# Optimization experiments

Measured on AMD Instinct MI355X. Metric: run time of the kernel, lower is better.

## Reference

```python
import jax, jax.numpy as jnp
import numpy as np

SEQ, D_A, H, D_K, D_V = 4096, 2048, 16, 128, 128


def setup_inputs() -> dict:
    key = jax.random.key(0)
    ks = jax.random.split(key, 7)
    return {
        "queries": jax.random.normal(ks[0], (SEQ, D_A), dtype=jnp.float32),
        "keys":    jax.random.normal(ks[1], (SEQ, D_A), dtype=jnp.float32),
        "values":  jax.random.normal(ks[2], (SEQ, D_A), dtype=jnp.float32),
        "Eq": jax.random.normal(ks[3], (H, D_A, D_K), dtype=jnp.float32),
        "Ek": jax.random.normal(ks[4], (H, D_A, D_K), dtype=jnp.float32),
        "Ev": jax.random.normal(ks[5], (H, D_A, D_V), dtype=jnp.float32),
        "W_out": jax.random.normal(ks[6], (H * D_V, D_A), dtype=jnp.float32),
    }


def reference(queries, keys, values, Eq, Ek, Ev, W_out):
    # Per-head projections: [seq, d_a] x [h, d_a, d] -> [h, seq, d]
    Q = jnp.einsum("sd,hdk->hsk", queries, Eq)
    K = jnp.einsum("sd,hdk->hsk", keys, Ek)
    V = jnp.einsum("sd,hdv->hsv", values, Ev)
    scale = 1.0 / D_K  # faithful to source: 1/d_k, not 1/sqrt(d_k)
    dots = jnp.einsum("hqk,hsk->hqs", Q, K) * scale  # [h, seq, seq]
    attn = jax.nn.softmax(dots, axis=-1)  # dropout p=0 -> identity
    out = jnp.einsum("hqs,hsv->hqv", attn, V)  # [h, seq, d_v]
    # concat heads along last dim: [seq, h*d_v]
    A = jnp.transpose(out, (1, 0, 2)).reshape(SEQ, H * D_V)
    return A @ W_out  # [seq, d_a]
```

## Files before the change

kernel.cpp:

```cpp
#include <hip/hip_runtime.h>

typedef unsigned short u16;
typedef __attribute__((ext_vector_type(4)))  float  f32x4;
typedef __attribute__((ext_vector_type(16))) float  f32x16;
typedef __attribute__((ext_vector_type(4)))  float  float4v;
typedef __attribute__((ext_vector_type(4)))  unsigned short u16x4;
typedef __attribute__((ext_vector_type(8)))  unsigned short u16x8;
typedef __attribute__((ext_vector_type(8)))  short s16x8;
typedef __attribute__((ext_vector_type(4)))  unsigned int u32x4;

#define SEQ 4096
#define DA  2048
#define NH  16
#define DKV 128

__device__ __forceinline__ u16 f2bf(float f) {
    unsigned u = __builtin_bit_cast(unsigned, f);
    u += 0x7FFFu + ((u >> 16) & 1u);
    return (u16)(u >> 16);
}
__device__ __forceinline__ float bf2f(u16 h) {
    return __builtin_bit_cast(float, (unsigned)h << 16);
}
__device__ __forceinline__ f32x4 mfma16(u16x8 a, u16x8 b, f32x4 c) {
    return __builtin_amdgcn_mfma_f32_16x16x32_bf16(
        __builtin_bit_cast(s16x8, a), __builtin_bit_cast(s16x8, b), c, 0, 0, 0);
}
__device__ __forceinline__ f32x16 mfma32(u16x8 a, u16x8 b, f32x16 c) {
    return __builtin_amdgcn_mfma_f32_32x32x16_bf16(
        __builtin_bit_cast(s16x8, a), __builtin_bit_cast(s16x8, b), c, 0, 0, 0);
}
__device__ __forceinline__ unsigned cvtpk(float lo, float hi) {
    unsigned r;
    asm("v_cvt_pk_bf16_f32 %0, %1, %2" : "=v"(r) : "v"(lo), "v"(hi));
    return r;
}
__device__ __forceinline__ char* ldsp(void* base, int row, int bcol, int rowbytes) {
    int off = row * rowbytes + bcol;
    off ^= (row & 7) << 4;
    return (char*)base + off;
}

__global__ void transpose_split_k(const float* __restrict__ in, u16* __restrict__ oh,
                                  u16* __restrict__ ol, int R, int C) {
    __shared__ float tile[32][33];
    int b  = blockIdx.z;
    int r0 = blockIdx.x * 32, c0 = blockIdx.y * 32;
    const float* src = in + (size_t)b * R * C;
    int t = threadIdx.x;
    {
        int cl = t & 31, r = t >> 5;
        for (int i = 0; i < 4; ++i)
            tile[r + 8 * i][cl] = src[(size_t)(r0 + r + 8 * i) * C + (c0 + cl)];
    }
    __syncthreads();
    int rl = t & 31, c = t >> 5;
    size_t obase = (size_t)b * R * C;
    for (int i = 0; i < 4; ++i) {
        int cw = c + 8 * i;
        float x = tile[rl][cw];
        u16 h = f2bf(x);
        size_t o = obase + (size_t)(c0 + cw) * R + (r0 + rl);
        oh[o] = h;
        if (ol) ol[o] = f2bf(x - bf2f(h));
    }
}

template <int MODE>
__global__ void __launch_bounds__(256) proj_k(const float* __restrict__ A,
                                              const u16* __restrict__ BTh,
                                              const u16* __restrict__ BTl,
                                              u16* __restrict__ Oh,
                                              u16* __restrict__ Ol) {
    __shared__ u16 sAh[128 * 64];
    __shared__ u16 sBh[128 * 64];
    __shared__ u16 sAl[MODE ? 128 * 64 : 8];
    __shared__ u16 sBl[MODE ? 128 * 64 : 8];

    int t = threadIdx.x;
    int h = blockIdx.y;
    int bm0 = blockIdx.x * 128;
    int lane = t & 63, w = t >> 6, wr = w >> 1, wc = w & 1;
    int g = lane >> 4, c = lane & 15;

    f32x4 acc[4][4] = {};

    for (int k0 = 0; k0 < DA; k0 += 64) {
        __syncthreads();
        for (int i = 0; i < 8; ++i) {
            int idx = t + i * 256;
            int row = idx >> 4, c4 = idx & 15;
            float4v av = *(const float4v*)(A + (size_t)(bm0 + row) * DA + k0 + c4 * 4);
            u16x4 hv, lv;
            for (int j = 0; j < 4; ++j) {
                u16 hh = f2bf(av[j]);
                hv[j] = hh;
                lv[j] = f2bf(av[j] - bf2f(hh));
            }
            *(u16x4*)ldsp(sAh, row, c4 * 8, 128) = hv;
            if (MODE) *(u16x4*)ldsp(sAl, row, c4 * 8, 128) = lv;
        }
        for (int i = 0; i < 4; ++i) {
            int idx = t + i * 256;
            int row = idx >> 3, c8 = idx & 7;
            size_t gb = ((size_t)h * 128 + row) * DA + k0 + c8 * 8;
            *(u16x8*)ldsp(sBh, row, c8 * 16, 128) = *(const u16x8*)(BTh + gb);
            if (MODE) *(u16x8*)ldsp(sBl, row, c8 * 16, 128) = *(const u16x8*)(BTl + gb);
        }
        __syncthreads();

        for (int kc = 0; kc < 2; ++kc) {
            int kb = (kc * 32 + g * 8) * 2;
            u16x8 ah[4], al[4], bh[4], bl[4];
            for (int m = 0; m < 4; ++m) {
                int row = wr * 64 + m * 16 + c;
                ah[m] = *(u16x8*)ldsp(sAh, row, kb, 128);
                if (MODE) al[m] = *(u16x8*)ldsp(sAl, row, kb, 128);
            }
            for (int n = 0; n < 4; ++n) {
                int row = wc * 64 + n * 16 + c;
                bh[n] = *(u16x8*)ldsp(sBh, row, kb, 128);
                if (MODE) bl[n] = *(u16x8*)ldsp(sBl, row, kb, 128);
            }
            for (int m = 0; m < 4; ++m)
                for (int n = 0; n < 4; ++n) {
                    acc[m][n] = mfma16(ah[m], bh[n], acc[m][n]);
                    if (MODE) {
                        acc[m][n] = mfma16(ah[m], bl[n], acc[m][n]);
                        acc[m][n] = mfma16(al[m], bh[n], acc[m][n]);
                    }
                }
        }
    }

    const float scale = (MODE == 2) ? (1.0f / 128.0f) : 1.0f;
    for (int m = 0; m < 4; ++m)
        for (int n = 0; n < 4; ++n) {
            int col  = wc * 64 + n * 16 + c;
            int row0 = bm0 + wr * 64 + m * 16 + g * 4;
            if (MODE == 0) {
                u16x4 pv;
                for (int j = 0; j < 4; ++j) pv[j] = f2bf(acc[m][n][j]);
                *(u16x4*)(Oh + ((size_t)h * DKV + col) * SEQ + row0) = pv;
            } else {
                for (int j = 0; j < 4; ++j) {
                    float v = acc[m][n][j] * scale;
                    u16 hh = f2bf(v);
                    size_t o = ((size_t)h * SEQ + row0 + j) * DKV + col;
                    Oh[o] = hh;
                    Ol[o] = f2bf(v - bf2f(hh));
                }
            }
        }
}

__global__ void __launch_bounds__(256, 2) attn_k(const u16* __restrict__ QH,
                                                 const u16* __restrict__ QL,
                                                 const u16* __restrict__ KH,
                                                 const u16* __restrict__ KL,
                                                 const u16* __restrict__ VT,
                                                 u16* __restrict__ Abuf) {
    __shared__ u16 sKh[64 * 128];
    __shared__ u16 sKl[64 * 128];
    __shared__ u16 sV[128 * 64];

    int t = threadIdx.x, lane = t & 63, w = t >> 6;
    int h = blockIdx.y, q0 = blockIdx.x * 128;
    int c = lane & 31, hi = lane >> 5;
    int qrow = q0 + w * 32 + c;

    u16x8 qh[8], ql[8];
    {
        size_t base = ((size_t)h * SEQ + qrow) * DKV + hi * 8;
#pragma unroll
        for (int dc = 0; dc < 8; ++dc) {
            qh[dc] = *(const u16x8*)(QH + base + dc * 16);
            ql[dc] = *(const u16x8*)(QL + base + dc * 16);
        }
    }

    f32x16 o[4] = {};
    float mrun = -3e38f, lrun = 0.f;

    for (int kv0 = 0; kv0 < SEQ; kv0 += 64) {
        __syncthreads();
#pragma unroll
        for (int i = 0; i < 4; ++i) {
            int idx = t + i * 256;
            {
                int row = idx >> 4, c8 = idx & 15;
                size_t gb = ((size_t)h * SEQ + kv0 + row) * DKV + c8 * 8;
                *(u16x8*)ldsp(sKh, row, c8 * 16, 256) = *(const u16x8*)(KH + gb);
                *(u16x8*)ldsp(sKl, row, c8 * 16, 256) = *(const u16x8*)(KL + gb);
            }
            {
                int row = idx >> 3, c8 = idx & 7;
                *(u16x8*)ldsp(sV, row, c8 * 16, 128) =
                    *(const u16x8*)(VT + ((size_t)h * DKV + row) * SEQ + kv0 + c8 * 8);
            }
        }
        __syncthreads();

        f32x16 s[2] = {};
        __builtin_amdgcn_s_setprio(1);
#pragma unroll
        for (int kt = 0; kt < 2; ++kt) {
#pragma unroll
            for (int dc = 0; dc < 8; ++dc) {
                u16x8 kh = *(u16x8*)ldsp(sKh, kt * 32 + c, dc * 32 + hi * 16, 256);
                u16x8 kl = *(u16x8*)ldsp(sKl, kt * 32 + c, dc * 32 + hi * 16, 256);
                s[kt] = mfma32(kh, qh[dc], s[kt]);
                s[kt] = mfma32(kl, qh[dc], s[kt]);
                s[kt] = mfma32(kh, ql[dc], s[kt]);
            }
        }
        __builtin_amdgcn_s_setprio(0);

        float vmax = s[0][0];
#pragma unroll
        for (int r = 1; r < 16; ++r) vmax = fmaxf(vmax, s[0][r]);
#pragma unroll
        for (int r = 0; r < 16; ++r) vmax = fmaxf(vmax, s[1][r]);
        vmax = fmaxf(vmax, __shfl_xor(vmax, 32));
        float mnew = fmaxf(mrun, vmax);
        float corr = __expf(mrun - mnew);
        mrun = mnew;
        float rs = 0.f;
#pragma unroll
        for (int kt = 0; kt < 2; ++kt)
#pragma unroll
            for (int r = 0; r < 16; ++r) {
                float p = __expf(s[kt][r] - mnew);
                s[kt][r] = p;
                rs += p;
            }
        rs += __shfl_xor(rs, 32);
        lrun = lrun * corr + rs;
#pragma unroll
        for (int vt = 0; vt < 4; ++vt)
#pragma unroll
            for (int r = 0; r < 16; ++r) o[vt][r] *= corr;

#pragma unroll
        for (int kt = 0; kt < 2; ++kt) {
            unsigned wv[8], xw[8];
#pragma unroll
            for (int i = 0; i < 8; ++i) wv[i] = cvtpk(s[kt][2 * i], s[kt][2 * i + 1]);
#pragma unroll
            for (int i = 0; i < 8; ++i) xw[i] = (unsigned)__shfl_xor((int)wv[i], 32);
            __builtin_amdgcn_s_setprio(1);
#pragma unroll
            for (int kc = 0; kc < 2; ++kc) {
                u32x4 pw;
                pw[0] = hi ? xw[4 * kc + 2] : wv[4 * kc + 0];
                pw[1] = hi ? xw[4 * kc + 3] : wv[4 * kc + 1];
                pw[2] = hi ? wv[4 * kc + 2] : xw[4 * kc + 0];
                pw[3] = hi ? wv[4 * kc + 3] : xw[4 * kc + 1];
                u16x8 pf = __builtin_bit_cast(u16x8, pw);
#pragma unroll
                for (int vt = 0; vt < 4; ++vt) {
                    u16x8 vf = *(u16x8*)ldsp(sV, vt * 32 + c, kt * 64 + kc * 32 + hi * 16, 128);
                    o[vt] = mfma32(vf, pf, o[vt]);
                }
            }
            __builtin_amdgcn_s_setprio(0);
        }
    }

    float inv = 1.0f / lrun;
#pragma unroll
    for (int vt = 0; vt < 4; ++vt)
#pragma unroll
        for (int rg = 0; rg < 4; ++rg) {
            u16x4 pv;
#pragma unroll
            for (int j = 0; j < 4; ++j) pv[j] = f2bf(o[vt][rg * 4 + j] * inv);
            *(u16x4*)(Abuf + (size_t)qrow * (NH * DKV) + h * DKV + vt * 32 + rg * 8 + hi * 4) = pv;
        }
}

__global__ void __launch_bounds__(256) gemm_out_k(const u16* __restrict__ Abuf,
                                                  const u16* __restrict__ WT,
                                                  float* __restrict__ out) {
    __shared__ u16 sA[128 * 64];
    __shared__ u16 sB[128 * 64];
    int t = threadIdx.x, lane = t & 63, w = t >> 6, wr = w >> 1, wc = w & 1;
    int g = lane >> 4, c = lane & 15;
    int bm0 = blockIdx.x * 128, bn0 = blockIdx.y * 128;
    f32x4 acc[4][4] = {};

    for (int k0 = 0; k0 < DA; k0 += 64) {
        __syncthreads();
        for (int i = 0; i < 4; ++i) {
            int idx = t + i * 256, row = idx >> 3, c8 = idx & 7;
            *(u16x8*)ldsp(sA, row, c8 * 16, 128) =
                *(const u16x8*)(Abuf + (size_t)(bm0 + row) * DA + k0 + c8 * 8);
            *(u16x8*)ldsp(sB, row, c8 * 16, 128) =
                *(const u16x8*)(WT + (size_t)(bn0 + row) * DA + k0 + c8 * 8);
        }
        __syncthreads();
        for (int kc = 0; kc < 2; ++kc) {
            int kb = (kc * 32 + g * 8) * 2;
            u16x8 af[4], bfq[4];
            for (int m = 0; m < 4; ++m) af[m]  = *(u16x8*)ldsp(sA, wr * 64 + m * 16 + c, kb, 128);
            for (int n = 0; n < 4; ++n) bfq[n] = *(u16x8*)ldsp(sB, wc * 64 + n * 16 + c, kb, 128);
            for (int m = 0; m < 4; ++m)
                for (int n = 0; n < 4; ++n)
                    acc[m][n] = mfma16(af[m], bfq[n], acc[m][n]);
        }
    }
    for (int m = 0; m < 4; ++m)
        for (int n = 0; n < 4; ++n) {
            int row0 = bm0 + wr * 64 + m * 16 + g * 4;
            int col  = bn0 + wc * 64 + n * 16 + c;
            for (int j = 0; j < 4; ++j)
                out[(size_t)(row0 + j) * DA + col] = acc[m][n][j];
        }
}

extern "C" void kernel_launch(void* const* d_in, const int* in_sizes, int n_in,
                              void* d_out, int out_size, void* d_ws, size_t ws_size,
                              hipStream_t stream) {
    const float* queries = (const float*)d_in[0];
    const float* keys    = (const float*)d_in[1];
    const float* values  = (const float*)d_in[2];
    const float* Eq      = (const float*)d_in[3];
    const float* Ek      = (const float*)d_in[4];
    const float* Ev      = (const float*)d_in[5];
    const float* Wout    = (const float*)d_in[6];
    float* out = (float*)d_out;

    const size_t PROJ = (size_t)NH * SEQ * DKV;
    const size_t TSZ  = (size_t)DA * DA;
    u16* p  = (u16*)d_ws;
    u16* QH = p; p += PROJ;
    u16* QL = p; p += PROJ;
    u16* KH = p; p += PROJ;
    u16* KL = p; p += PROJ;
    u16* VT = p; p += PROJ;
    u16* AB = p; p += (size_t)SEQ * NH * DKV;
    u16* TH = p; p += TSZ;
    u16* TL = p; p += TSZ;

    dim3 tgE(DA / 32, DKV / 32, NH);
    dim3 tgW(DA / 32, DA / 32, 1);
    dim3 pg(SEQ / 128, NH);

    transpose_split_k<<<tgE, 256, 0, stream>>>(Eq, TH, TL, DA, DKV);
    proj_k<2><<<pg, 256, 0, stream>>>(queries, TH, TL, QH, QL);
    transpose_split_k<<<tgE, 256, 0, stream>>>(Ek, TH, TL, DA, DKV);
    proj_k<1><<<pg, 256, 0, stream>>>(keys, TH, TL, KH, KL);
    transpose_split_k<<<tgE, 256, 0, stream>>>(Ev, TH, nullptr, DA, DKV);
    proj_k<0><<<pg, 256, 0, stream>>>(values, TH, nullptr, VT, nullptr);
    transpose_split_k<<<tgW, 256, 0, stream>>>(Wout, TH, nullptr, DA, DA);
    attn_k<<<dim3(SEQ / 128, NH), 256, 0, stream>>>(QH, QL, KH, KL, VT, AB);
    gemm_out_k<<<dim3(SEQ / 128, DA / 128), 256, 0, stream>>>(AB, TH, out);
}
```

Before: 675.4 us.

## Register-prefetch next tiles in projection, attention and output GEMM kernels

Each of the three main kernels now loads the next K-tile from global memory into registers right after the LDS barrier, so the global-load latency overlaps the MFMA work on the current tile. The registers are written to LDS at the start of the next iteration. Launch bounds on the projection and output GEMM kernels also request two blocks per SM. This adds register pressure and one redundant wrap-around prefetch at the final iteration, and the occupancy hint may force spills.

```diff
diff --git a/kernel.cpp b/kernel.cpp
--- a/kernel.cpp
+++ b/kernel.cpp
@@ -67,11 +67,11 @@
 }
 
 template <int MODE>
-__global__ void __launch_bounds__(256) proj_k(const float* __restrict__ A,
-                                              const u16* __restrict__ BTh,
-                                              const u16* __restrict__ BTl,
-                                              u16* __restrict__ Oh,
-                                              u16* __restrict__ Ol) {
+__global__ void __launch_bounds__(256, 2) proj_k(const float* __restrict__ A,
+                                                 const u16* __restrict__ BTh,
+                                                 const u16* __restrict__ BTl,
+                                                 u16* __restrict__ Oh,
+                                                 u16* __restrict__ Ol) {
     __shared__ u16 sAh[128 * 64];
     __shared__ u16 sBh[128 * 64];
     __shared__ u16 sAl[MODE ? 128 * 64 : 8];
@@ -85,29 +85,56 @@
 
     f32x4 acc[4][4] = {};
 
-    for (int k0 = 0; k0 < DA; k0 += 64) {
-        __syncthreads();
+    float4v pA[8];
+    u16x8   pBh[4], pBl[4];
+
+    auto prefetch = [&](int k0) {
+#pragma unroll
         for (int i = 0; i < 8; ++i) {
             int idx = t + i * 256;
             int row = idx >> 4, c4 = idx & 15;
-            float4v av = *(const float4v*)(A + (size_t)(bm0 + row) * DA + k0 + c4 * 4);
+            pA[i] = *(const float4v*)(A + (size_t)(bm0 + row) * DA + k0 + c4 * 4);
+        }
+#pragma unroll
+        for (int i = 0; i < 4; ++i) {
+            int idx = t + i * 256;
+            int row = idx >> 3, c8 = idx & 7;
+            size_t gb = ((size_t)h * 128 + row) * DA + k0 + c8 * 8;
+            pBh[i] = *(const u16x8*)(BTh + gb);
+            if (MODE) pBl[i] = *(const u16x8*)(BTl + gb);
+        }
+    };
+    auto write_lds = [&]() {
+#pragma unroll
+        for (int i = 0; i < 8; ++i) {
+            int idx = t + i * 256;
+            int row = idx >> 4, c4 = idx & 15;
             u16x4 hv, lv;
+#pragma unroll
             for (int j = 0; j < 4; ++j) {
-                u16 hh = f2bf(av[j]);
+                u16 hh = f2bf(pA[i][j]);
                 hv[j] = hh;
-                lv[j] = f2bf(av[j] - bf2f(hh));
+                lv[j] = f2bf(pA[i][j] - bf2f(hh));
             }
             *(u16x4*)ldsp(sAh, row, c4 * 8, 128) = hv;
             if (MODE) *(u16x4*)ldsp(sAl, row, c4 * 8, 128) = lv;
         }
+#pragma unroll
         for (int i = 0; i < 4; ++i) {
             int idx = t + i * 256;
             int row = idx >> 3, c8 = idx & 7;
-            size_t gb = ((size_t)h * 128 + row) * DA + k0 + c8 * 8;
-            *(u16x8*)ldsp(sBh, row, c8 * 16, 128) = *(const u16x8*)(BTh + gb);
-            if (MODE) *(u16x8*)ldsp(sBl, row, c8 * 16, 128) = *(const u16x8*)(BTl + gb);
-        }
-        __syncthreads();
+            *(u16x8*)ldsp(sBh, row, c8 * 16, 128) = pBh[i];
+            if (MODE) *(u16x8*)ldsp(sBl, row, c8 * 16, 128) = pBl[i];
+        }
+    };
+
+    prefetch(0);
+    for (int k0 = 0; k0 < DA; k0 += 64) {
+        __syncthreads();
+        write_lds();
+        __syncthreads();
+        int nxt = (k0 + 64 < DA) ? k0 + 64 : 0;
+        prefetch(nxt);
 
         for (int kc = 0; kc < 2; ++kc) {
             int kb = (kc * 32 + g * 8) * 2;
@@ -182,24 +209,38 @@
     f32x16 o[4] = {};
     float mrun = -3e38f, lrun = 0.f;
 
+    u16x8 pkh[4], pkl[4], pvv[4];
+    auto prefetch = [&](int kv) {
+#pragma unroll
+        for (int i = 0; i < 4; ++i) {
+            int idx = t + i * 256;
+            int rowK = idx >> 4, c8K = idx & 15;
+            size_t gb = ((size_t)h * SEQ + kv + rowK) * DKV + c8K * 8;
+            pkh[i] = *(const u16x8*)(KH + gb);
+            pkl[i] = *(const u16x8*)(KL + gb);
+            int rowV = idx >> 3, c8V = idx & 7;
+            pvv[i] = *(const u16x8*)(VT + ((size_t)h * DKV + rowV) * SEQ + kv + c8V * 8);
+        }
+    };
+    auto write_lds = [&]() {
+#pragma unroll
+        for (int i = 0; i < 4; ++i) {
+            int idx = t + i * 256;
+            int rowK = idx >> 4, c8K = idx & 15;
+            *(u16x8*)ldsp(sKh, rowK, c8K * 16, 256) = pkh[i];
+            *(u16x8*)ldsp(sKl, rowK, c8K * 16, 256) = pkl[i];
+            int rowV = idx >> 3, c8V = idx & 7;
+            *(u16x8*)ldsp(sV, rowV, c8V * 16, 128) = pvv[i];
+        }
+    };
+
+    prefetch(0);
     for (int kv0 = 0; kv0 < SEQ; kv0 += 64) {
         __syncthreads();
-#pragma unroll
-        for (int i = 0; i < 4; ++i) {
-            int idx = t + i * 256;
-            {
-                int row = idx >> 4, c8 = idx & 15;
-                size_t gb = ((size_t)h * SEQ + kv0 + row) * DKV + c8 * 8;
-                *(u16x8*)ldsp(sKh, row, c8 * 16, 256) = *(const u16x8*)(KH + gb);
-                *(u16x8*)ldsp(sKl, row, c8 * 16, 256) = *(const u16x8*)(KL + gb);
-            }
-            {
-                int row = idx >> 3, c8 = idx & 7;
-                *(u16x8*)ldsp(sV, row, c8 * 16, 128) =
-                    *(const u16x8*)(VT + ((size_t)h * DKV + row) * SEQ + kv0 + c8 * 8);
-            }
-        }
-        __syncthreads();
+        write_lds();
+        __syncthreads();
+        int nxt = (kv0 + 64 < SEQ) ? kv0 + 64 : 0;
+        prefetch(nxt);
 
         f32x16 s[2] = {};
         __builtin_amdgcn_s_setprio(1);
@@ -279,9 +320,9 @@
         }
 }
 
-__global__ void __launch_bounds__(256) gemm_out_k(const u16* __restrict__ Abuf,
-                                                  const u16* __restrict__ WT,
-                                                  float* __restrict__ out) {
+__global__ void __launch_bounds__(256, 2) gemm_out_k(const u16* __restrict__ Abuf,
+                                                     const u16* __restrict__ WT,
+                                                     float* __restrict__ out) {
     __shared__ u16 sA[128 * 64];
     __shared__ u16 sB[128 * 64];
     int t = threadIdx.x, lane = t & 63, w = t >> 6, wr = w >> 1, wc = w & 1;
@@ -289,16 +330,32 @@
     int bm0 = blockIdx.x * 128, bn0 = blockIdx.y * 128;
     f32x4 acc[4][4] = {};
 
+    u16x8 pA[4], pB[4];
+    auto prefetch = [&](int k0) {
+#pragma unroll
+        for (int i = 0; i < 4; ++i) {
+            int idx = t + i * 256, row = idx >> 3, c8 = idx & 7;
+            pA[i] = *(const u16x8*)(Abuf + (size_t)(bm0 + row) * DA + k0 + c8 * 8);
+            pB[i] = *(const u16x8*)(WT + (size_t)(bn0 + row) * DA + k0 + c8 * 8);
+        }
+    };
+    auto write_lds = [&]() {
+#pragma unroll
+        for (int i = 0; i < 4; ++i) {
+            int idx = t + i * 256, row = idx >> 3, c8 = idx & 7;
+            *(u16x8*)ldsp(sA, row, c8 * 16, 128) = pA[i];
+            *(u16x8*)ldsp(sB, row, c8 * 16, 128) = pB[i];
+        }
+    };
+
+    prefetch(0);
     for (int k0 = 0; k0 < DA; k0 += 64) {
         __syncthreads();
-        for (int i = 0; i < 4; ++i) {
-            int idx = t + i * 256, row = idx >> 3, c8 = idx & 7;
-            *(u16x8*)ldsp(sA, row, c8 * 16, 128) =
-                *(const u16x8*)(Abuf + (size_t)(bm0 + row) * DA + k0 + c8 * 8);
-            *(u16x8*)ldsp(sB, row, c8 * 16, 128) =
-                *(const u16x8*)(WT + (size_t)(bn0 + row) * DA + k0 + c8 * 8);
-        }
-        __syncthreads();
+        write_lds();
+        __syncthreads();
+        int nxt = (k0 + 64 < DA) ? k0 + 64 : 0;
+        prefetch(nxt);
+
         for (int kc = 0; kc < 2; ++kc) {
             int kb = (kc * 32 + g * 8) * 2;
             u16x8 af[4], bfq[4];
```

Measured after the change: 686.0 us. About the same (+1.6%).
